# Kernel optimization log

Measured on AMD Instinct MI355X. Metric: run time of the kernel, lower is better.

Reference implementation:

```python
import jax, jax.numpy as jnp
import numpy as np

B, N, M, V, H, K = 32, 9, 128, 512, 256, 8
TYPES, PAD, TAU = 21, 0, 1.0
NS, NT = N - 1, TYPES - 9  # span slots (2..N), type slots (9..TYPES-1)


def setup_inputs() -> dict:
    key = jax.random.key(0)
    ks = jax.random.split(key, 6)
    decodings = jax.random.normal(ks[0], (B, N, M, V), jnp.float32)
    target_types = jax.random.randint(ks[1], (B,), 9, TYPES)
    spans = jax.random.randint(ks[2], (B,), 2, N + 1)
    type_emb = jax.random.normal(ks[3], (TYPES, H), jnp.float32)
    dec_sem_W = jax.random.normal(ks[4], (NS, NT, K * (N + 1), H), jnp.float32) / np.sqrt(H).astype(np.float32)
    dec_sem_b = jnp.zeros((NS, NT, K * (N + 1)), jnp.float32)
    u = jax.random.uniform(ks[5], (B, K, N + 1), jnp.float32, 1e-10, 1.0)
    gumbel = -jnp.log(-jnp.log(u))
    return dict(decodings=decodings, type_emb=type_emb, dec_sem_W=dec_sem_W,
                dec_sem_b=dec_sem_b, gumbel=gumbel,
                target_types=target_types, spans=spans)


def reference(decodings, type_emb, dec_sem_W, dec_sem_b, gumbel, target_types, spans):
    # --- per-sample template logits: decoder_sem[span-2][type-9](type_embedding) ---
    emb = type_emb[target_types]                           # (B, H)
    Wi = dec_sem_W[spans - 2, target_types - 9]            # (B, K*(N+1), H)
    bi = dec_sem_b[spans - 2, target_types - 9]            # (B, K*(N+1))
    logits = (jnp.einsum('boh,bh->bo', Wi, emb) + bi).reshape(B, K, N + 1)
    pos = jnp.arange(N + 1)
    valid = pos[None, None, :] <= spans[:, None, None]     # first span+1 slots only
    logits = jnp.where(valid, logits, -1e30)
    logp = jax.nn.log_softmax(logits, -1)
    # gumbel_softmax(hard=True), straight-through
    y_soft = jax.nn.softmax((logp + gumbel) / TAU, -1)
    y_hard = jax.nn.one_hot(jnp.argmax(y_soft, -1), N + 1, dtype=y_soft.dtype)
    dt = y_hard + y_soft - jax.lax.stop_gradient(y_soft)
    dt = jnp.where(valid, dt, 0.0)
    # type == 20 uses the fixed start template (row 0 picks decoding 0, rest pad)
    start = jnp.zeros((K, N + 1)).at[0, 1].set(1.0).at[1:, 0].set(1.0)
    dt = jnp.where((target_types == 20)[:, None, None], start[None], dt)

    # --- apply_decoder_template, vectorized over batch ---
    pad_row = jnp.tile(jax.nn.one_hot(PAD, V, dtype=decodings.dtype), M)  # (M*V,)
    pos_m = jnp.arange(M)

    def per_sample(dt_i, dec_i):
        choices = jnp.concatenate([pad_row[None], dec_i.reshape(N, M * V)], 0)  # (N+1, M*V)
        out = (dt_i @ choices).reshape(K, M, V)            # (K, M, V)
        idxs = jnp.argmax(out, -1)                         # (K, M)
        raw_len = jnp.max(jnp.where(idxs != PAD, pos_m + 1, 0), axis=1)  # (K,)
        ends = jnp.minimum(jnp.cumsum(raw_len), M)
        starts = jnp.concatenate([jnp.zeros(1, ends.dtype), ends[:-1]])
        lens = ends - starts                               # sequential clipped concat
        dest = starts[:, None] + pos_m[None]
        ok = pos_m[None] < lens[:, None]
        dest = jnp.where(ok, dest, M)                      # dump invalid writes in row M
        res = jnp.zeros((M + 1, V), out.dtype).at[dest.reshape(-1)].add(
            out.reshape(K * M, V) * ok.reshape(-1, 1))
        return res[:M]

    new_d = jax.vmap(per_sample)(dt, decodings)            # (B, M, V)
    new_v = jnp.zeros((B, 20, 3, V), decodings.dtype)
    return new_d, new_v
```

## Files before the change

kernel.cpp:

```cpp
#include <hip/hip_runtime.h>

#define B 32
#define N 9
#define M 128
#define V 512
#define H 256
#define K 8
#define NT 12
#define NP1 10
#define SPLITS 8
#define ROWS_PER_SPLIT 16
#define SCAN_BLKS (B*N*SPLITS)
#define SEL_BLKS (B*K)
#define NEWV_ROWS (B*20*3)

__device__ __forceinline__ float wave_sum(float v) {
    #pragma unroll
    for (int off = 32; off > 0; off >>= 1) v += __shfl_xor(v, off, 64);
    return v;
}

__global__ __launch_bounds__(256) void k_scan_sel(
    const float* __restrict__ dec, const float* __restrict__ type_emb,
    const float* __restrict__ W, const float* __restrict__ bias,
    const float* __restrict__ gumbel, const int* __restrict__ types,
    const int* __restrict__ spans,
    int* __restrict__ jstar, int* __restrict__ part)
{
    const int blk = blockIdx.x;
    const int t = threadIdx.x, wave = t >> 6, lane = t & 63;

    if (blk < SCAN_BLKS) {
        const int s  = blk & (SPLITS - 1);
        const int bs = blk >> 3;
        const int b = bs / N, slab = bs % N;
        const int typ = types[b], span = spans[b];
        if (slab >= span) return;
        if (typ == 20 && slab != 0) return;

        const float* src = dec + (long)bs * M * V;
        int best = 0;
        const int m0 = s * ROWS_PER_SPLIT + wave * 4;
        #pragma unroll
        for (int i = 0; i < 4; ++i) {
            const int m = m0 + i;
            const float4* row = (const float4*)(src + (long)m * V);
            float4 a = row[lane];
            float4 c = row[lane + 64];
            float x0 = __shfl(a.x, 0, 64);
            float loc = (lane == 0) ? fmaxf(fmaxf(a.y, a.z), a.w)
                                    : fmaxf(fmaxf(a.x, a.y), fmaxf(a.z, a.w));
            loc = fmaxf(loc, fmaxf(fmaxf(c.x, c.y), fmaxf(c.z, c.w)));
            if (__ballot(loc > x0)) best = m + 1;
        }
        __shared__ int bs_s[4];
        if (lane == 0) bs_s[wave] = best;
        __syncthreads();
        if (t == 0)
            part[blk] = max(max(bs_s[0], bs_s[1]), max(bs_s[2], bs_s[3]));
    } else {
        const int bk = blk - SCAN_BLKS;
        const int b = bk >> 3, k = bk & 7;
        const int typ = types[b], span = spans[b];
        __shared__ float logits_s[NP1];

        const long base = ((long)(span - 2) * NT + (typ - 9)) * (K * NP1) + k * NP1;
        const float4 e4 = ((const float4*)(type_emb + typ * H))[lane];
        for (int j = wave; j < NP1; j += 4) {
            const float4 w4 = ((const float4*)(W + (base + j) * H))[lane];
            float ssum = w4.x * e4.x + w4.y * e4.y + w4.z * e4.z + w4.w * e4.w;
            ssum = wave_sum(ssum);
            if (lane == 0)
                logits_s[j] = ssum + bias[base + j] + gumbel[bk * NP1 + j];
        }
        __syncthreads();
        if (t == 0) {
            int bj = 0;
            if (typ == 20) {
                bj = (k == 0) ? 1 : 0;
            } else {
                float bestv = -3.0e38f;
                for (int j = 0; j <= span; ++j) {
                    const float v = logits_s[j];
                    if (v > bestv) { bestv = v; bj = j; }
                }
            }
            jstar[bk] = bj;
        }
    }
}

__global__ __launch_bounds__(256) void k_write(
    const float* __restrict__ dec, const int* __restrict__ jstar,
    const int* __restrict__ part, float* __restrict__ out)
{
    const int blk = blockIdx.x;
    const int t = threadIdx.x;
    const int half = t >> 7, t1 = t & 127;

    if (blk >= B * (M / 2)) {
        const int r = (blk - B * (M / 2)) * 2 + half;
        float4* dst = (float4*)(out + (long)B * M * V + (long)r * V);
        dst[t1] = make_float4(0.f, 0.f, 0.f, 0.f);
        return;
    }

    const int b = blk >> 6;
    const int m = ((blk & 63) << 1) + half;

    int found_k = -1, src_m = 0, cum = 0;
    #pragma unroll
    for (int k = 0; k < K; ++k) {
        const int j = jstar[b * K + k];
        int rl = 0;
        if (j > 0) {
            const int* p = part + ((b * N + (j - 1)) << 3);
            #pragma unroll
            for (int q = 0; q < SPLITS; ++q) rl = max(rl, p[q]);
        }
        const int e = min(cum + rl, M);
        if (found_k < 0 && m < e) { found_k = k; src_m = m - cum; }
        cum = e;
    }

    float4* dst = (float4*)(out + ((long)b * M + m) * V);
    if (found_k < 0) {
        dst[t1] = make_float4(0.f, 0.f, 0.f, 0.f);
    } else {
        const int j = jstar[b * K + found_k];
        const float4* src = (const float4*)(dec + ((long)(b * N + (j - 1)) * M + src_m) * V);
        dst[t1] = src[t1];
    }
}

extern "C" void kernel_launch(void* const* d_in, const int* in_sizes, int n_in,
                              void* d_out, int out_size, void* d_ws, size_t ws_size,
                              hipStream_t stream) {
    const float* dec      = (const float*)d_in[0];
    const float* type_emb = (const float*)d_in[1];
    const float* W        = (const float*)d_in[2];
    const float* bias     = (const float*)d_in[3];
    const float* gumbel   = (const float*)d_in[4];
    const int*   types    = (const int*)d_in[5];
    const int*   spans    = (const int*)d_in[6];
    float* out = (float*)d_out;

    int* jstar = (int*)d_ws;
    int* part  = jstar + B * K;

    k_scan_sel<<<SCAN_BLKS + SEL_BLKS, 256, 0, stream>>>(
        dec, type_emb, W, bias, gumbel, types, spans, jstar, part);
    k_write<<<B * (M / 2) + NEWV_ROWS / 2, 256, 0, stream>>>(dec, jstar, part, out);
}
```

Before: 123.0 us.

## Scan slabs backward with early exit and move new_v zeroing into first kernel

The raw-length scan now uses one block per (batch, slab) and walks 16-row chunks from the end of the sequence. It stops at the first chunk that holds a row whose argmax is not PAD, so it avoids reading whole slabs when the last rows are non-pad, which is the usual case for random data. This removes the per-split partial results and their reduction in the write kernel. The zero-fill of the new_v output moves from the write kernel into the scan/select kernel. The cost is fewer, serialized blocks with a __syncthreads per chunk, so parallelism drops when slabs are mostly pad.

```diff
diff --git a/kernel.cpp b/kernel.cpp
--- a/kernel.cpp
+++ b/kernel.cpp
@@ -8,11 +8,11 @@
 #define K 8
 #define NT 12
 #define NP1 10
-#define SPLITS 8
-#define ROWS_PER_SPLIT 16
-#define SCAN_BLKS (B*N*SPLITS)
+#define CHUNK 16
+#define SCAN_BLKS (B*N)
 #define SEL_BLKS (B*K)
 #define NEWV_ROWS (B*20*3)
+#define NEWV_BLKS (NEWV_ROWS/2)
 
 __device__ __forceinline__ float wave_sum(float v) {
     #pragma unroll
@@ -25,40 +25,46 @@
     const float* __restrict__ W, const float* __restrict__ bias,
     const float* __restrict__ gumbel, const int* __restrict__ types,
     const int* __restrict__ spans,
-    int* __restrict__ jstar, int* __restrict__ part)
+    int* __restrict__ jstar, int* __restrict__ part, float* __restrict__ out)
 {
     const int blk = blockIdx.x;
     const int t = threadIdx.x, wave = t >> 6, lane = t & 63;
 
     if (blk < SCAN_BLKS) {
-        const int s  = blk & (SPLITS - 1);
-        const int bs = blk >> 3;
+        const int bs = blk;
         const int b = bs / N, slab = bs % N;
         const int typ = types[b], span = spans[b];
         if (slab >= span) return;
         if (typ == 20 && slab != 0) return;
 
         const float* src = dec + (long)bs * M * V;
-        int best = 0;
-        const int m0 = s * ROWS_PER_SPLIT + wave * 4;
-        #pragma unroll
-        for (int i = 0; i < 4; ++i) {
-            const int m = m0 + i;
-            const float4* row = (const float4*)(src + (long)m * V);
-            float4 a = row[lane];
-            float4 c = row[lane + 64];
-            float x0 = __shfl(a.x, 0, 64);
-            float loc = (lane == 0) ? fmaxf(fmaxf(a.y, a.z), a.w)
-                                    : fmaxf(fmaxf(a.x, a.y), fmaxf(a.z, a.w));
-            loc = fmaxf(loc, fmaxf(fmaxf(c.x, c.y), fmaxf(c.z, c.w)));
-            if (__ballot(loc > x0)) best = m + 1;
+        __shared__ int chunk_best;
+        for (int c = 0; c < M / CHUNK; ++c) {
+            if (t == 0) chunk_best = 0;
+            __syncthreads();
+            const int mbase = M - CHUNK * (c + 1) + wave * (CHUNK / 4);
+            int best = 0;
+            #pragma unroll
+            for (int i = 0; i < CHUNK / 4; ++i) {
+                const int m = mbase + i;
+                const float4* row = (const float4*)(src + (long)m * V);
+                float4 a = row[lane];
+                float4 c4 = row[lane + 64];
+                float x0 = __shfl(a.x, 0, 64);
+                float loc = (lane == 0) ? fmaxf(fmaxf(a.y, a.z), a.w)
+                                        : fmaxf(fmaxf(a.x, a.y), fmaxf(a.z, a.w));
+                loc = fmaxf(loc, fmaxf(fmaxf(c4.x, c4.y), fmaxf(c4.z, c4.w)));
+                if (__ballot(loc > x0)) best = m + 1;
+            }
+            if (lane == 0 && best) atomicMax(&chunk_best, best);
+            __syncthreads();
+            if (chunk_best) {
+                if (t == 0) part[bs] = chunk_best;
+                return;
+            }
         }
-        __shared__ int bs_s[4];
-        if (lane == 0) bs_s[wave] = best;
-        __syncthreads();
-        if (t == 0)
-            part[blk] = max(max(bs_s[0], bs_s[1]), max(bs_s[2], bs_s[3]));
-    } else {
+        if (t == 0) part[bs] = 0;
+    } else if (blk < SCAN_BLKS + SEL_BLKS) {
         const int bk = blk - SCAN_BLKS;
         const int b = bk >> 3, k = bk & 7;
         const int typ = types[b], span = spans[b];
@@ -87,6 +93,11 @@
             }
             jstar[bk] = bj;
         }
+    } else {
+        const int half = t >> 7, t1 = t & 127;
+        const int r = (blk - SCAN_BLKS - SEL_BLKS) * 2 + half;
+        float4* dst = (float4*)(out + (long)B * M * V + (long)r * V);
+        dst[t1] = make_float4(0.f, 0.f, 0.f, 0.f);
     }
 }
 
@@ -98,13 +109,6 @@
     const int t = threadIdx.x;
     const int half = t >> 7, t1 = t & 127;
 
-    if (blk >= B * (M / 2)) {
-        const int r = (blk - B * (M / 2)) * 2 + half;
-        float4* dst = (float4*)(out + (long)B * M * V + (long)r * V);
-        dst[t1] = make_float4(0.f, 0.f, 0.f, 0.f);
-        return;
-    }
-
     const int b = blk >> 6;
     const int m = ((blk & 63) << 1) + half;
 
@@ -112,12 +116,7 @@
     #pragma unroll
     for (int k = 0; k < K; ++k) {
         const int j = jstar[b * K + k];
-        int rl = 0;
-        if (j > 0) {
-            const int* p = part + ((b * N + (j - 1)) << 3);
-            #pragma unroll
-            for (int q = 0; q < SPLITS; ++q) rl = max(rl, p[q]);
-        }
+        const int rl = (j > 0) ? part[b * N + (j - 1)] : 0;
         const int e = min(cum + rl, M);
         if (found_k < 0 && m < e) { found_k = k; src_m = m - cum; }
         cum = e;
@@ -148,7 +147,7 @@
     int* jstar = (int*)d_ws;
     int* part  = jstar + B * K;
 
-    k_scan_sel<<<SCAN_BLKS + SEL_BLKS, 256, 0, stream>>>(
-        dec, type_emb, W, bias, gumbel, types, spans, jstar, part);
-    k_write<<<B * (M / 2) + NEWV_ROWS / 2, 256, 0, stream>>>(dec, jstar, part, out);
+    k_scan_sel<<<SCAN_BLKS + SEL_BLKS + NEWV_BLKS, 256, 0, stream>>>(
+        dec, type_emb, W, bias, gumbel, types, spans, jstar, part, out);
+    k_write<<<B * (M / 2), 256, 0, stream>>>(dec, jstar, part, out);
 }
```

Result: faster. 118.5 us (-3.7%).
